# Kernel tuning notes

Hardware: AMD Instinct MI355X
Metric: run time of the kernel (lower is better)

Reference implementation:

```python
import jax, jax.numpy as jnp
import numpy as np

B, P, S = 32, 4096, 128
D_INT, D_VC, D_PATCH, H = 512, 512, 768, 4
D_CONCAT = D_INT + D_VC
D_HEAD = D_CONCAT // H  # 256
TEMPERATURE = 1.0


def setup_inputs() -> dict:
    key = jax.random.key(0)
    ks = jax.random.split(key, 9)
    h_int = jax.random.normal(ks[0], (B, D_INT), dtype=jnp.float32)
    h_vc = jax.random.normal(ks[1], (B, D_VC), dtype=jnp.float32)
    patch_tokens = jax.random.normal(ks[2], (B, P, D_PATCH), dtype=jnp.float32)
    boundaries = jnp.sort(jax.random.randint(ks[3], (S + 1,), 0, P, dtype=jnp.int32))
    # Per-head projection weights (nn.Linear: y = x @ W.T + b)
    qW = jax.random.normal(ks[4], (H, D_HEAD, D_CONCAT), dtype=jnp.float32) / np.sqrt(D_CONCAT)
    qb = jax.random.normal(ks[5], (H, D_HEAD), dtype=jnp.float32) * 0.01
    kW = jax.random.normal(ks[6], (H, D_HEAD, D_PATCH), dtype=jnp.float32) / np.sqrt(D_PATCH)
    kb = jax.random.normal(ks[7], (H, D_HEAD), dtype=jnp.float32) * 0.01
    return {"h_int": h_int, "h_vc": h_vc, "patch_tokens": patch_tokens,
            "boundaries": boundaries, "qW": qW, "qb": qb, "kW": kW, "kb": kb}


def reference(h_int, h_vc, patch_tokens, boundaries, qW, qb, kW, kb):
    b, p, _ = patch_tokens.shape
    s = boundaries.shape[0] - 1
    h_concat = jnp.concatenate([h_int, h_vc], axis=-1)            # [B, d_concat]
    # All heads at once (equivalent to the per-head Python loop)
    q = jnp.einsum('bc,hdc->bhd', h_concat, qW) + qb              # [B, H, d_head]
    k = jnp.einsum('bpc,hdc->bphd', patch_tokens, kW) + kb        # [B, P, H, d_head]
    patch_scores = jnp.einsum('bhd,bphd->bph', q, k)              # [B, P, H]
    # Map each patch to its stroke segment; out-of-range -> dump bucket s
    pos = jnp.arange(p)
    seg = jnp.searchsorted(boundaries, pos, side='right') - 1     # [P]
    seg = jnp.where((seg < 0) | (seg >= s), s, seg)
    st = patch_scores.transpose(1, 0, 2)                          # [P, B, H]
    ssum = jax.ops.segment_sum(st, seg, num_segments=s + 1)[:s]   # [S, B, H]
    cnt = jax.ops.segment_sum(jnp.ones((p,), st.dtype), seg, num_segments=s + 1)[:s]  # [S]
    stroke_scores = ssum / jnp.maximum(cnt, 1.0)[:, None, None]   # mean over patches; 0 if empty
    avg_scores = stroke_scores.mean(axis=-1).transpose(1, 0)      # [B, S] (mean over heads)
    return jax.nn.sigmoid(avg_scores / TEMPERATURE)
```

## Files before the change

kernel.cpp:

```cpp
#include <hip/hip_runtime.h>
#include <math.h>

#define NB 32
#define NP 4096
#define NS 128
#define DI 512
#define DV 512
#define DP 768
#define NH 4
#define DC 1024
#define DH 256

typedef float f4 __attribute__((ext_vector_type(4)));

__global__ __launch_bounds__(256) void k_qw(const float* __restrict__ h_int,
                                            const float* __restrict__ h_vc,
                                            const float* __restrict__ qW,
                                            const float* __restrict__ qb,
                                            const float* __restrict__ kW,
                                            const float* __restrict__ kb,
                                            float* __restrict__ w_part,
                                            float* __restrict__ bavg_part,
                                            float* __restrict__ acc) {
    int b = blockIdx.x / NH, h = blockIdx.x % NH;
    int tid = threadIdx.x;

    int g = blockIdx.x * 256 + tid;
    if (g < NB * (NS + 1)) acc[g] = 0.f;

    __shared__ float hc[DC];
    __shared__ float qs[DH];
    for (int i = tid; i < DI; i += 256) hc[i] = h_int[b * DI + i];
    for (int i = tid; i < DV; i += 256) hc[DI + i] = h_vc[b * DV + i];
    __syncthreads();

    const float* w = qW + (size_t)(h * DH + tid) * DC;
    float acc_q = qb[h * DH + tid];
#pragma unroll 8
    for (int c = 0; c < DC; c += 4) {
        f4 wv = *(const f4*)(w + c);
        acc_q += wv.x * hc[c] + wv.y * hc[c + 1] + wv.z * hc[c + 2] + wv.w * hc[c + 3];
    }
    qs[tid] = acc_q;
    __syncthreads();

    const float inv_h = 1.0f / NH;
    if (tid < DP / 4) {
        f4 wacc = 0.f;
        const float* kbase = kW + (size_t)(h * DH) * DP + 4 * tid;
#pragma unroll 8
        for (int i = 0; i < DH; ++i) {
            f4 kv = *(const f4*)(kbase + (size_t)i * DP);
            wacc += qs[i] * kv;
        }
        *(f4*)(w_part + (size_t)(b * NH + h) * DP + 4 * tid) = wacc * inv_h;
    }

    float pb = qs[tid] * kb[h * DH + tid];
#pragma unroll
    for (int off = 32; off > 0; off >>= 1) pb += __shfl_xor(pb, off);
    __shared__ float red[4];
    int wave = tid >> 6, lane = tid & 63;
    if (lane == 0) red[wave] = pb;
    __syncthreads();
    if (tid == 0) bavg_part[b * NH + h] = (red[0] + red[1] + red[2] + red[3]) * inv_h;
}

__global__ __launch_bounds__(256, 4) void k_score(const float* __restrict__ patch,
                                                  const float* __restrict__ w_part,
                                                  const int* __restrict__ bnd,
                                                  float* __restrict__ acc) {
    constexpr int CHUNKS = 32;
    constexpr int PPB = NP / CHUNKS;
    constexpr int PPW = PPB / 4;
    constexpr int RS = DP / 4;
    int b = blockIdx.x / CHUNKS;
    int chunk = blockIdx.x % CHUNKS;
    __shared__ int bsh[NS + 1];
    int tid = threadIdx.x;
    if (tid <= NS) bsh[tid] = bnd[tid];
    __syncthreads();
    int wave = tid >> 6, lane = tid & 63;

    const f4* wp = (const f4*)(w_part + (size_t)b * NH * DP);
    f4 w0 = 0.f, w1 = 0.f, w2 = 0.f;
#pragma unroll
    for (int h = 0; h < NH; ++h) {
        w0 += wp[h * RS + lane];
        w1 += wp[h * RS + 64 + lane];
        w2 += wp[h * RS + 128 + lane];
    }
    float* accb = acc + (size_t)b * (NS + 1);

    int p0 = chunk * PPB + wave * PPW;

    int cur, nxt;
    if (p0 < bsh[0]) {
        cur = NS; nxt = bsh[0];
    } else {
        int lo = 0, hi = NS;
        while (lo < hi) {
            int mid = (lo + hi + 1) >> 1;
            if (bsh[mid] <= p0) lo = mid; else hi = mid - 1;
        }
        cur = lo;
        nxt = (cur < NS) ? bsh[cur + 1] : NP;
    }

    f4 r0 = 0.f, r1 = 0.f, r2 = 0.f;
    const f4* base = (const f4*)(patch + ((size_t)b * NP + p0) * DP);

#define LOADROW(dst0, dst1, dst2, i)                                          \
    {                                                                         \
        const f4* rp_ = base + (size_t)(i) * RS;                              \
        dst0 = __builtin_nontemporal_load(rp_ + lane);                        \
        dst1 = __builtin_nontemporal_load(rp_ + 64 + lane);                   \
        dst2 = __builtin_nontemporal_load(rp_ + 128 + lane);                  \
    }

#define PROCROW(s0, s1, s2, i)                                                \
    {                                                                         \
        int p_ = p0 + (i);                                                    \
        if (p_ >= nxt) {        \
            f4 sv = r0 * w0 + r1 * w1 + r2 * w2;                              \
            float s = sv.x + sv.y + sv.z + sv.w;                              \
            for (int off_ = 32; off_ > 0; off_ >>= 1) s += __shfl_xor(s, off_); \
            if (lane == 0) atomicAdd(&accb[cur], s);                          \
            r0 = 0.f; r1 = 0.f; r2 = 0.f;                                     \
            cur = (cur == NS) ? 0 : cur + 1;                                  \
            while (cur < NS && bsh[cur + 1] <= p_) cur++;                     \
            nxt = (cur < NS) ? bsh[cur + 1] : NP;                             \
        }                                                                     \
        r0 += s0; r1 += s1; r2 += s2;                                         \
    }

    f4 A0, A1, A2, B0, B1, B2, C0, C1, C2, D0, D1, D2;
    LOADROW(A0, A1, A2, 0)
    LOADROW(B0, B1, B2, 1)
#pragma unroll
    for (int g2 = 0; g2 < PPW - 2; g2 += 2) {
        LOADROW(C0, C1, C2, g2 + 2)
        LOADROW(D0, D1, D2, g2 + 3)
        PROCROW(A0, A1, A2, g2)
        PROCROW(B0, B1, B2, g2 + 1)
        A0 = C0; A1 = C1; A2 = C2;
        B0 = D0; B1 = D1; B2 = D2;
    }
    PROCROW(A0, A1, A2, PPW - 2)
    PROCROW(B0, B1, B2, PPW - 1)

    {
        f4 sv = r0 * w0 + r1 * w1 + r2 * w2;
        float s = sv.x + sv.y + sv.z + sv.w;
#pragma unroll
        for (int off = 32; off > 0; off >>= 1) s += __shfl_xor(s, off);
        if (lane == 0) atomicAdd(&accb[cur], s);
    }
#undef LOADROW
#undef PROCROW
}

__global__ __launch_bounds__(256) void k_out(const float* __restrict__ acc,
                                             const float* __restrict__ bavg_part,
                                             const int* __restrict__ bnd,
                                             float* __restrict__ out) {
    int i = blockIdx.x * 256 + threadIdx.x;
    if (i >= NB * NS) return;
    int b = i / NS, s = i % NS;
    int cnt = bnd[s + 1] - bnd[s];
    float v = 0.f;
    if (cnt > 0) {
        float bb = bavg_part[b * NH] + bavg_part[b * NH + 1]
                 + bavg_part[b * NH + 2] + bavg_part[b * NH + 3];
        v = acc[b * (NS + 1) + s] / (float)cnt + bb;
    }
    out[i] = 1.0f / (1.0f + expf(-v));
}

extern "C" void kernel_launch(void* const* d_in, const int* in_sizes, int n_in,
                              void* d_out, int out_size, void* d_ws, size_t ws_size,
                              hipStream_t stream) {
    const float* h_int = (const float*)d_in[0];
    const float* h_vc  = (const float*)d_in[1];
    const float* patch = (const float*)d_in[2];
    const int*   bnd   = (const int*)d_in[3];
    const float* qW    = (const float*)d_in[4];
    const float* qb    = (const float*)d_in[5];
    const float* kW    = (const float*)d_in[6];
    const float* kb    = (const float*)d_in[7];
    float* out = (float*)d_out;

    float* acc       = (float*)d_ws;
    float* w_part    = acc + NB * (NS + 1);
    float* bavg_part = w_part + NB * NH * DP;

    k_qw<<<NB * NH, 256, 0, stream>>>(h_int, h_vc, qW, qb, kW, kb,
                                      w_part, bavg_part, acc);
    k_score<<<NB * 32, 256, 0, stream>>>(patch, w_part, bnd, acc);
    k_out<<<(NB * NS + 255) / 256, 256, 0, stream>>>(acc, bavg_part, bnd, out);
}
```

Before: 108.1 us.

## Split query/weight precompute into two kernels with finer-grained parallel blocks

The fused q-projection and q·kW kernel is split into two kernels. k_q2 uses 512 blocks, with four threads per output reducing a quarter of the input each, to compute q and partial bias terms. k_w2 uses 384 blocks, each computing a 256-column slice of the folded weight vector with a shared-memory reduction over row chunks. The aim is to raise parallelism and latency hiding in the serial prologue that ran on only 128 blocks, at the cost of one extra launch and a round trip of q through global memory.

```diff
diff --git a/kernel.cpp b/kernel.cpp
--- a/kernel.cpp
+++ b/kernel.cpp
@@ -13,57 +13,81 @@
 
 typedef float f4 __attribute__((ext_vector_type(4)));
 
-__global__ __launch_bounds__(256) void k_qw(const float* __restrict__ h_int,
+__global__ __launch_bounds__(256) void k_q2(const float* __restrict__ h_int,
                                             const float* __restrict__ h_vc,
                                             const float* __restrict__ qW,
                                             const float* __restrict__ qb,
-                                            const float* __restrict__ kW,
                                             const float* __restrict__ kb,
-                                            float* __restrict__ w_part,
+                                            float* __restrict__ q,
                                             float* __restrict__ bavg_part,
                                             float* __restrict__ acc) {
-    int b = blockIdx.x / NH, h = blockIdx.x % NH;
+    int b = blockIdx.x >> 4, g = blockIdx.x & 15;
     int tid = threadIdx.x;
 
-    int g = blockIdx.x * 256 + tid;
-    if (g < NB * (NS + 1)) acc[g] = 0.f;
+    int zi = blockIdx.x * 256 + tid;
+    if (zi < NB * (NS + 1)) acc[zi] = 0.f;
 
     __shared__ float hc[DC];
-    __shared__ float qs[DH];
     for (int i = tid; i < DI; i += 256) hc[i] = h_int[b * DI + i];
     for (int i = tid; i < DV; i += 256) hc[DI + i] = h_vc[b * DV + i];
     __syncthreads();
 
-    const float* w = qW + (size_t)(h * DH + tid) * DC;
-    float acc_q = qb[h * DH + tid];
+    int j = tid >> 2, r = tid & 3;
+    int o = g * 64 + j;
+    const float* w = qW + (size_t)o * DC + r * 256;
+    const float* hq = hc + r * 256;
+    float s = 0.f;
 #pragma unroll 8
-    for (int c = 0; c < DC; c += 4) {
+    for (int c = 0; c < 256; c += 4) {
         f4 wv = *(const f4*)(w + c);
-        acc_q += wv.x * hc[c] + wv.y * hc[c + 1] + wv.z * hc[c + 2] + wv.w * hc[c + 3];
-    }
-    qs[tid] = acc_q;
-    __syncthreads();
-
-    const float inv_h = 1.0f / NH;
-    if (tid < DP / 4) {
-        f4 wacc = 0.f;
-        const float* kbase = kW + (size_t)(h * DH) * DP + 4 * tid;
+        s += wv.x * hq[c] + wv.y * hq[c + 1] + wv.z * hq[c + 2] + wv.w * hq[c + 3];
+    }
+    s += __shfl_xor(s, 1);
+    s += __shfl_xor(s, 2);
+    float qv = s + qb[o];
+
+    __shared__ float red[64];
+    if (r == 0) {
+        q[(size_t)b * (NH * DH) + o] = qv;
+        red[j] = qv * kb[o];
+    }
+    __syncthreads();
+    if (tid == 0) {
+        float t = 0.f;
+        for (int i = 0; i < 64; ++i) t += red[i];
+        bavg_part[b * 16 + g] = t;
+    }
+}
+
+__global__ __launch_bounds__(256) void k_w2(const float* __restrict__ q,
+                                            const float* __restrict__ kW,
+                                            float* __restrict__ w_part) {
+    int bid = blockIdx.x;
+    int cc = bid % 3, bh = bid / 3;
+    int h = bh % NH, b = bh / NH;
+    int tid = threadIdx.x;
+
+    __shared__ float qs[DH];
+    __shared__ f4 part[4][64];
+    if (tid < DH) qs[tid] = q[(size_t)b * (NH * DH) + h * DH + tid];
+    __syncthreads();
+
+    int rc = tid >> 6, cg = tid & 63;
+    const float* kbase = kW + (size_t)(h * DH + rc * 64) * DP + cc * 256 + cg * 4;
+    const float* qr = qs + rc * 64;
+    f4 wacc = 0.f;
 #pragma unroll 8
-        for (int i = 0; i < DH; ++i) {
-            f4 kv = *(const f4*)(kbase + (size_t)i * DP);
-            wacc += qs[i] * kv;
-        }
-        *(f4*)(w_part + (size_t)(b * NH + h) * DP + 4 * tid) = wacc * inv_h;
-    }
-
-    float pb = qs[tid] * kb[h * DH + tid];
-#pragma unroll
-    for (int off = 32; off > 0; off >>= 1) pb += __shfl_xor(pb, off);
-    __shared__ float red[4];
-    int wave = tid >> 6, lane = tid & 63;
-    if (lane == 0) red[wave] = pb;
-    __syncthreads();
-    if (tid == 0) bavg_part[b * NH + h] = (red[0] + red[1] + red[2] + red[3]) * inv_h;
+    for (int i = 0; i < 64; ++i) {
+        f4 kv = *(const f4*)(kbase + (size_t)i * DP);
+        wacc += qr[i] * kv;
+    }
+    part[rc][cg] = wacc;
+    __syncthreads();
+    if (rc == 0) {
+        f4 t = (part[0][cg] + part[1][cg]) + (part[2][cg] + part[3][cg]);
+        *(f4*)(w_part + (size_t)(b * NH + h) * DP + cc * 256 + cg * 4) =
+            t * (1.0f / NH);
+    }
 }
 
 __global__ __launch_bounds__(256, 4) void k_score(const float* __restrict__ patch,
@@ -170,9 +194,10 @@
     int cnt = bnd[s + 1] - bnd[s];
     float v = 0.f;
     if (cnt > 0) {
-        float bb = bavg_part[b * NH] + bavg_part[b * NH + 1]
-                 + bavg_part[b * NH + 2] + bavg_part[b * NH + 3];
-        v = acc[b * (NS + 1) + s] / (float)cnt + bb;
+        float bb = 0.f;
+#pragma unroll
+        for (int g = 0; g < 16; ++g) bb += bavg_part[b * 16 + g];
+        v = acc[b * (NS + 1) + s] / (float)cnt + bb * (1.0f / NH);
     }
     out[i] = 1.0f / (1.0f + expf(-v));
 }
@@ -193,9 +218,10 @@
     float* acc       = (float*)d_ws;
     float* w_part    = acc + NB * (NS + 1);
     float* bavg_part = w_part + NB * NH * DP;
-
-    k_qw<<<NB * NH, 256, 0, stream>>>(h_int, h_vc, qW, qb, kW, kb,
-                                      w_part, bavg_part, acc);
+    float* q         = bavg_part + NB * 16;
+
+    k_q2<<<NB * 16, 256, 0, stream>>>(h_int, h_vc, qW, qb, kb, q, bavg_part, acc);
+    k_w2<<<NB * NH * 3, 256, 0, stream>>>(q, kW, w_part);
     k_score<<<NB * 32, 256, 0, stream>>>(patch, w_part, bnd, acc);
     k_out<<<(NB * NS + 255) / 256, 256, 0, stream>>>(acc, bavg_part, bnd, out);
 }
```

New measurement: 92.34 us, median of 2. 1.17x faster.
